# Performance work log

Measured on AMD Instinct MI355X. Metric: run time of the kernel, lower is better.

## Reference

```python
import jax, jax.numpy as jnp
import numpy as np

N = 100000  # nodes
E = 1600000  # directed edges

_DIMS = [("eg1", 3, 160), ("eg2", 160, 80), ("eg3", 80, 40), ("eg4", 40, 20),
         ("el1", 20, 10), ("el2", 10, 3), ("dl1", 3, 10), ("dl2", 10, 20),
         ("dg1", 20, 40), ("dg2", 40, 80), ("dg3", 80, 160), ("dg4", 160, 3)]


def _lin_init(key, ci, co):
    s = 1.0 / np.sqrt(ci)
    kw, kb = jax.random.split(key)
    w = jax.random.uniform(kw, (ci, co), jnp.float32, -s, s)
    b = jax.random.uniform(kb, (co,), jnp.float32, -s, s)
    return w, b


def setup_inputs():
    key = jax.random.key(0)
    k0, k1, k2 = jax.random.split(key, 3)
    x = jax.random.normal(k0, (N, 3), jnp.float32)
    src = jax.random.randint(k1, (E,), 0, N)
    dst = jax.random.randint(k2, (E,), 0, N)
    edge_index = jnp.stack([src, dst])  # [2, E] int32 indices
    out = {"x": x, "edge_index": edge_index}
    for i, (name, ci, co) in enumerate(_DIMS):
        w, b = _lin_init(jax.random.fold_in(key, i + 10), ci, co)
        out[name + "_w"] = w
        out[name + "_b"] = b
    return out


def _gcn(x, w, b, src, dst, norm):
    # PyG GCNConv: linear transform, then symmetric-normalized scatter-add.
    h = x @ w
    agg = jax.ops.segment_sum(h[src] * norm[:, None], dst, num_segments=N)
    return agg + b


def reference(x, edge_index, eg1_w, eg1_b, eg2_w, eg2_b, eg3_w, eg3_b, eg4_w, eg4_b,
              el1_w, el1_b, el2_w, el2_b, dl1_w, dl1_b, dl2_w, dl2_b,
              dg1_w, dg1_b, dg2_w, dg2_b, dg3_w, dg3_b, dg4_w, dg4_b):
    loops = jnp.arange(N)
    src = jnp.concatenate([edge_index[0], loops])  # add self-loops (PyG default)
    dst = jnp.concatenate([edge_index[1], loops])
    deg = jax.ops.segment_sum(jnp.ones(src.shape[0], x.dtype), dst, num_segments=N)
    dis = jnp.where(deg > 0, jax.lax.rsqrt(deg), 0.0)
    norm = dis[src] * dis[dst]  # D^-1/2 A D^-1/2 edge weights
    relu = jax.nn.relu
    h = relu(_gcn(x, eg1_w, eg1_b, src, dst, norm))
    h = relu(_gcn(h, eg2_w, eg2_b, src, dst, norm))
    h = relu(_gcn(h, eg3_w, eg3_b, src, dst, norm))
    h = relu(_gcn(h, eg4_w, eg4_b, src, dst, norm))
    h = relu(h @ el1_w + el1_b)
    h = h @ el2_w + el2_b  # latent [N, 3]
    h = relu(h @ dl1_w + dl1_b)
    h = relu(h @ dl2_w + dl2_b)
    h = relu(_gcn(h, dg1_w, dg1_b, src, dst, norm))
    h = relu(_gcn(h, dg2_w, dg2_b, src, dst, norm))
    h = relu(_gcn(h, dg3_w, dg3_b, src, dst, norm))
    h = jnp.tanh(_gcn(h, dg4_w, dg4_b, src, dst, norm))
    return h
```

## Files before the change

### kernel.cpp

```cpp
#include <hip/hip_runtime.h>
#include <hip/hip_fp16.h>
#include <math.h>

#define BS 256
static constexpr int NN = 100000;
static constexpr int EE = 1600000;
static constexpr int BUCKET_SH = 7;
static constexpr int NBUCKET = (NN + 127) >> BUCKET_SH;
static constexpr int NB_PART = 256;
static constexpr int CHUNK = EE / NB_PART;
static constexpr int NP = NBUCKET * NB_PART;
static constexpr int SCAN_ELEMS = 1024;
static constexpr int NPB = (NP + SCAN_ELEMS - 1) / SCAN_ELEMS;

static inline int cdiv(long long a, int b) { return (int)((a + b - 1) / b); }

template <int ACT>
__device__ __forceinline__ float act_f(float v) {
    if (ACT == 1) return fmaxf(v, 0.0f);
    if (ACT == 2) return tanhf(v);
    return v;
}

__device__ __forceinline__ unsigned short h16(float v) {
    return __half_as_ushort(__float2half(v));
}
__device__ __forceinline__ unsigned pack2h(float a, float b) {
    return (unsigned)h16(a) | ((unsigned)h16(b) << 16);
}
__device__ __forceinline__ float4 cvt4h(uint2 r) {
    float2 fa = __half22float2(*(const __half2*)&r.x);
    float2 fb = __half22float2(*(const __half2*)&r.y);
    return make_float4(fa.x, fa.y, fb.x, fb.y);
}
__device__ __forceinline__ void acc8h(uint4 r, float4& a, float4& b) {
    float2 f0 = __half22float2(*(const __half2*)&r.x);
    float2 f1 = __half22float2(*(const __half2*)&r.y);
    float2 f2 = __half22float2(*(const __half2*)&r.z);
    float2 f3 = __half22float2(*(const __half2*)&r.w);
    a.x += f0.x; a.y += f0.y; a.z += f1.x; a.w += f1.y;
    b.x += f2.x; b.y += f2.y; b.z += f3.x; b.w += f3.y;
}

template <int OUTM>
__device__ __forceinline__ void store1(float* out, size_t idx, float v, float dn) {
    if (OUTM == 0) out[idx] = v;
    else if (OUTM == 1) out[idx] = v * dn;
    else if (OUTM == 2) ((unsigned short*)out)[idx] = h16(v * dn);
    else ((unsigned short*)out)[idx] = h16(v);
}

__global__ __launch_bounds__(256) void k_hist(const int* __restrict__ dst,
                                              int* __restrict__ part_cnt) {
    __shared__ int h[NBUCKET];
    int b = blockIdx.x;
    for (int j = threadIdx.x; j < NBUCKET; j += 256) h[j] = 0;
    __syncthreads();
    int e0 = b * CHUNK;
    for (int k = threadIdx.x; k < CHUNK; k += 256)
        atomicAdd(&h[dst[e0 + k] >> BUCKET_SH], 1);
    __syncthreads();
    for (int j = threadIdx.x; j < NBUCKET; j += 256)
        part_cnt[j * NB_PART + b] = h[j];
}

__global__ void k_scanA(const int* __restrict__ in, int* __restrict__ outp,
                        int* __restrict__ bsums) {
    __shared__ int lds[BS];
    int base = blockIdx.x * SCAN_ELEMS;
    int t = threadIdx.x;
    int v[4];
    int s = 0;
#pragma unroll
    for (int j = 0; j < 4; ++j) {
        int idx = base + t * 4 + j;
        v[j] = (idx < NP) ? in[idx] : 0;
        s += v[j];
    }
    lds[t] = s;
    __syncthreads();
    for (int off = 1; off < BS; off <<= 1) {
        int add = (t >= off) ? lds[t - off] : 0;
        __syncthreads();
        lds[t] += add;
        __syncthreads();
    }
    int run = lds[t] - s;
    if (t == BS - 1) bsums[blockIdx.x] = lds[BS - 1];
#pragma unroll
    for (int j = 0; j < 4; ++j) {
        int idx = base + t * 4 + j;
        if (idx < NP) outp[idx] = run;
        run += v[j];
    }
}

__global__ void k_scanB(int* __restrict__ bsums) {
    if (threadIdx.x == 0 && blockIdx.x == 0) {
        int acc = 0;
        for (int i = 0; i < NPB; ++i) {
            int t = bsums[i];
            bsums[i] = acc;
            acc += t;
        }
    }
}

__global__ void k_scanC(int* __restrict__ outp, const int* __restrict__ bsums,
                        int* __restrict__ bbase) {
    int i = blockIdx.x * BS + threadIdx.x;
    if (i < NP) {
        int v = outp[i] + bsums[i / SCAN_ELEMS];
        outp[i] = v;
        if ((i & (NB_PART - 1)) == 0) bbase[i / NB_PART] = v;
    }
    if (i == 0) bbase[NBUCKET] = EE;
}

__global__ __launch_bounds__(256) void k_part(const int* __restrict__ src,
                                              const int* __restrict__ dst,
                                              const int* __restrict__ scan_out,
                                              unsigned* __restrict__ epb) {
    __shared__ int cur[NBUCKET];
    int b = blockIdx.x;
    for (int j = threadIdx.x; j < NBUCKET; j += 256) cur[j] = scan_out[j * NB_PART + b];
    __syncthreads();
    int e0 = b * CHUNK;
    for (int k = threadIdx.x; k < CHUNK; k += 256) {
        int e = e0 + k;
        int d = dst[e];
        int s = src[e];
        int pos = atomicAdd(&cur[d >> BUCKET_SH], 1);
        epb[pos] = ((unsigned)(d & ((1 << BUCKET_SH) - 1)) << 17) | (unsigned)s;
    }
}

__global__ __launch_bounds__(256) void k_fine2(const int* __restrict__ bbase,
                                               const unsigned* __restrict__ epb,
                                               int* __restrict__ eidx,
                                               int* __restrict__ rowptr,
                                               float* __restrict__ dis) {
    __shared__ int hcnt[1 << BUCKET_SH];
    __shared__ int hoff[1 << BUCKET_SH];
    int b = blockIdx.x;
    int n0 = b << BUCKET_SH;
    int nloc = min(1 << BUCKET_SH, NN - n0);
    int t = threadIdx.x;
    if (t < (1 << BUCKET_SH)) hcnt[t] = 0;
    __syncthreads();
    int es = bbase[b], ee = bbase[b + 1];
    for (int k = es + t; k < ee; k += 256) atomicAdd(&hcnt[epb[k] >> 17], 1);
    __syncthreads();
    if (t < (1 << BUCKET_SH)) hoff[t] = hcnt[t];
    __syncthreads();
    for (int off = 1; off < (1 << BUCKET_SH); off <<= 1) {
        int add = (t >= off && t < (1 << BUCKET_SH)) ? hoff[t - off] : 0;
        __syncthreads();
        if (t < (1 << BUCKET_SH)) hoff[t] += add;
        __syncthreads();
    }
    if (t < nloc) {
        int excl = hoff[t] - hcnt[t];
        rowptr[n0 + t] = es + excl;
        dis[n0 + t] = rsqrtf((float)(hcnt[t] + 1));
    }
    __syncthreads();
    if (t < (1 << BUCKET_SH)) hoff[t] = es + hoff[t] - hcnt[t];
    __syncthreads();
    for (int k = es + t; k < ee; k += 256) {
        unsigned p = epb[k];
        int pos = atomicAdd(&hoff[p >> 17], 1);
        eidx[pos] = (int)(p & 0x1FFFFu);
    }
    if (b == NBUCKET - 1 && t == 0) rowptr[NN] = EE;
}

template <int C, int ACT, bool HASB, bool OUTH>
__global__ void k_gatherw(const unsigned short* __restrict__ g, const int* __restrict__ rowptr,
                          const int* __restrict__ eidx, const float* __restrict__ dis,
                          const float* __restrict__ b, float* __restrict__ out) {
    static_assert(C % 8 == 0, "C%8");
    constexpr int V = C / 8;
    int t = blockIdx.x * BS + threadIdx.x;
    if (t >= NN * V) return;
    int n = t / V, v = t % V;
    const uint4* g4 = (const uint4*)g;
    float4 accA = make_float4(0.f, 0.f, 0.f, 0.f);
    float4 accB = make_float4(0.f, 0.f, 0.f, 0.f);
    acc8h(g4[(size_t)n * V + v], accA, accB);
    int rs = rowptr[n], re = rowptr[n + 1];
    int k = rs;
    for (; k + 4 <= re; k += 4) {
        int s0 = eidx[k + 0], s1 = eidx[k + 1], s2 = eidx[k + 2], s3 = eidx[k + 3];
        uint4 r0 = g4[(size_t)s0 * V + v];
        uint4 r1 = g4[(size_t)s1 * V + v];
        uint4 r2 = g4[(size_t)s2 * V + v];
        uint4 r3 = g4[(size_t)s3 * V + v];
        acc8h(r0, accA, accB);
        acc8h(r1, accA, accB);
        acc8h(r2, accA, accB);
        acc8h(r3, accA, accB);
    }
    for (; k < re; ++k) {
        acc8h(g4[(size_t)eidx[k] * V + v], accA, accB);
    }
    float dn = dis[n];
    accA.x *= dn; accA.y *= dn; accA.z *= dn; accA.w *= dn;
    accB.x *= dn; accB.y *= dn; accB.z *= dn; accB.w *= dn;
    if (HASB) {
        float4 b0 = ((const float4*)b)[v * 2 + 0];
        float4 b1 = ((const float4*)b)[v * 2 + 1];
        accA.x += b0.x; accA.y += b0.y; accA.z += b0.z; accA.w += b0.w;
        accB.x += b1.x; accB.y += b1.y; accB.z += b1.z; accB.w += b1.w;
    }
    accA.x = act_f<ACT>(accA.x); accA.y = act_f<ACT>(accA.y);
    accA.z = act_f<ACT>(accA.z); accA.w = act_f<ACT>(accA.w);
    accB.x = act_f<ACT>(accB.x); accB.y = act_f<ACT>(accB.y);
    accB.z = act_f<ACT>(accB.z); accB.w = act_f<ACT>(accB.w);
    if (OUTH) {
        uint4 u;
        u.x = pack2h(accA.x, accA.y);
        u.y = pack2h(accA.z, accA.w);
        u.z = pack2h(accB.x, accB.y);
        u.w = pack2h(accB.z, accB.w);
        ((uint4*)out)[(size_t)n * V + v] = u;
    } else {
        float4* op = (float4*)out + (size_t)n * (C / 4) + v * 2;
        op[0] = accA;
        op[1] = accB;
    }
}

template <int C, int ACT, bool HASB, bool OUTH>
__global__ void k_gatherh(const unsigned short* __restrict__ g, const int* __restrict__ rowptr,
                          const int* __restrict__ eidx, const float* __restrict__ dis,
                          const float* __restrict__ b, float* __restrict__ out) {
    static_assert(C % 4 == 0, "C%4");
    constexpr int V = C / 4;
    int t = blockIdx.x * BS + threadIdx.x;
    if (t >= NN * V) return;
    int n = t / V, v = t % V;
    const uint2* g2 = (const uint2*)g;
    float4 acc = cvt4h(g2[(size_t)n * V + v]);
    int rs = rowptr[n], re = rowptr[n + 1];
    int k = rs;
    for (; k + 4 <= re; k += 4) {
        int s0 = eidx[k + 0], s1 = eidx[k + 1], s2 = eidx[k + 2], s3 = eidx[k + 3];
        uint2 r0 = g2[(size_t)s0 * V + v];
        uint2 r1 = g2[(size_t)s1 * V + v];
        uint2 r2 = g2[(size_t)s2 * V + v];
        uint2 r3 = g2[(size_t)s3 * V + v];
        float4 h0 = cvt4h(r0), h1 = cvt4h(r1), h2 = cvt4h(r2), h3 = cvt4h(r3);
        acc.x += (h0.x + h1.x) + (h2.x + h3.x);
        acc.y += (h0.y + h1.y) + (h2.y + h3.y);
        acc.z += (h0.z + h1.z) + (h2.z + h3.z);
        acc.w += (h0.w + h1.w) + (h2.w + h3.w);
    }
    for (; k < re; ++k) {
        float4 hv = cvt4h(g2[(size_t)eidx[k] * V + v]);
        acc.x += hv.x; acc.y += hv.y; acc.z += hv.z; acc.w += hv.w;
    }
    float dn = dis[n];
    acc.x *= dn; acc.y *= dn; acc.z *= dn; acc.w *= dn;
    if (HASB) {
        float4 bb = ((const float4*)b)[v];
        acc.x += bb.x; acc.y += bb.y; acc.z += bb.z; acc.w += bb.w;
    }
    acc.x = act_f<ACT>(acc.x);
    acc.y = act_f<ACT>(acc.y);
    acc.z = act_f<ACT>(acc.z);
    acc.w = act_f<ACT>(acc.w);
    if (OUTH) {
        uint2 u;
        u.x = pack2h(acc.x, acc.y);
        u.y = pack2h(acc.z, acc.w);
        ((uint2*)out)[(size_t)n * V + v] = u;
    } else {
        ((float4*)out)[(size_t)n * V + v] = acc;
    }
}

template <int ACT, bool HASB>
__global__ void k_gather3d(const float* __restrict__ g, const int* __restrict__ rowptr,
                           const int* __restrict__ eidx, const float* __restrict__ dis,
                           const float* __restrict__ b, float* __restrict__ out) {
    int n = blockIdx.x * BS + threadIdx.x;
    if (n >= NN) return;
    const float* gp = g + (size_t)n * 3;
    float a0 = gp[0], a1 = gp[1], a2 = gp[2];
    int rs = rowptr[n], re = rowptr[n + 1];
    int k = rs;
    for (; k + 4 <= re; k += 4) {
        const float* q0 = g + (size_t)eidx[k + 0] * 3;
        const float* q1 = g + (size_t)eidx[k + 1] * 3;
        const float* q2 = g + (size_t)eidx[k + 2] * 3;
        const float* q3 = g + (size_t)eidx[k + 3] * 3;
        float b00 = q0[0], b01 = q0[1], b02 = q0[2];
        float b10 = q1[0], b11 = q1[1], b12 = q1[2];
        float b20 = q2[0], b21 = q2[1], b22 = q2[2];
        float b30 = q3[0], b31 = q3[1], b32 = q3[2];
        a0 += (b00 + b10) + (b20 + b30);
        a1 += (b01 + b11) + (b21 + b31);
        a2 += (b02 + b12) + (b22 + b32);
    }
    for (; k < re; ++k) {
        const float* gq = g + (size_t)eidx[k] * 3;
        a0 += gq[0]; a1 += gq[1]; a2 += gq[2];
    }
    float dn = dis[n];
    a0 *= dn; a1 *= dn; a2 *= dn;
    if (HASB) { a0 += b[0]; a1 += b[1]; a2 += b[2]; }
    float* op = out + (size_t)n * 3;
    op[0] = act_f<ACT>(a0);
    op[1] = act_f<ACT>(a1);
    op[2] = act_f<ACT>(a2);
}

__global__ void k_scale3(const float* __restrict__ x, const float* __restrict__ dis,
                         float* __restrict__ g) {
    int i = blockIdx.x * BS + threadIdx.x;
    if (i < NN * 3) g[i] = x[i] * dis[i / 3];
}

__global__ __launch_bounds__(256) void k_latent(const unsigned short* __restrict__ in20,
                                                const float* __restrict__ el1_w, const float* __restrict__ el1_b,
                                                const float* __restrict__ el2_w, const float* __restrict__ el2_b,
                                                const float* __restrict__ dl1_w, const float* __restrict__ dl1_b,
                                                const float* __restrict__ dl2_w, const float* __restrict__ dl2_b,
                                                const float* __restrict__ dis,
                                                unsigned short* __restrict__ G) {
    __shared__ float w1[200], b1[10], w2[30], b2[3], w3[30], b3[10], w4[200], b4[20];
    int t = threadIdx.x;
    if (t < 200) w1[t] = el1_w[t];
    if (t < 10) b1[t] = el1_b[t];
    if (t < 30) w2[t] = el2_w[t];
    if (t < 3) b2[t] = el2_b[t];
    if (t < 30) w3[t] = dl1_w[t];
    if (t < 10) b3[t] = dl1_b[t];
    if (t < 200) w4[t] = dl2_w[t];
    if (t < 20) b4[t] = dl2_b[t];
    __syncthreads();
    int n = blockIdx.x * 256 + t;
    if (n >= NN) return;
    float h0[20];
    const uint2* ip = (const uint2*)in20 + (size_t)n * 5;
#pragma unroll
    for (int v = 0; v < 5; ++v) {
        float4 f = cvt4h(ip[v]);
        h0[v * 4 + 0] = f.x; h0[v * 4 + 1] = f.y;
        h0[v * 4 + 2] = f.z; h0[v * 4 + 3] = f.w;
    }
    float a1[10];
#pragma unroll
    for (int j = 0; j < 10; ++j) {
        float s = b1[j];
#pragma unroll
        for (int i = 0; i < 20; ++i) s = fmaf(h0[i], w1[i * 10 + j], s);
        a1[j] = fmaxf(s, 0.0f);
    }
    float a2[3];
#pragma unroll
    for (int j = 0; j < 3; ++j) {
        float s = b2[j];
#pragma unroll
        for (int i = 0; i < 10; ++i) s = fmaf(a1[i], w2[i * 3 + j], s);
        a2[j] = s;
    }
    float a3[10];
#pragma unroll
    for (int j = 0; j < 10; ++j) {
        float s = b3[j];
#pragma unroll
        for (int i = 0; i < 3; ++i) s = fmaf(a2[i], w3[i * 10 + j], s);
        a3[j] = fmaxf(s, 0.0f);
    }
    float dn = dis[n];
    uint2* gp = (uint2*)G + (size_t)n * 5;
#pragma unroll
    for (int v = 0; v < 5; ++v) {
        float o[4];
#pragma unroll
        for (int q = 0; q < 4; ++q) {
            int j = v * 4 + q;
            float s = b4[j];
#pragma unroll
            for (int i = 0; i < 10; ++i) s = fmaf(a3[i], w4[i * 20 + j], s);
            o[q] = fmaxf(s, 0.0f) * dn;
        }
        uint2 u;
        u.x = pack2h(o[0], o[1]);
        u.y = pack2h(o[2], o[3]);
        gp[v] = u;
    }
}

template <int CIN, int COUT, int TC, int TN, int TM, int BK, int ACT, bool HASB, int OUTM, bool INH>
__global__ __launch_bounds__(256) void k_mm_tiled(const float* __restrict__ x,
                                                  const float* __restrict__ w,
                                                  const float* __restrict__ b,
                                                  float* __restrict__ out,
                                                  const float* __restrict__ dis) {
    constexpr int TR = 256 / TC;
    constexpr int BM = TR * TM;
    constexpr int LDA = BM + 4;
    constexpr int CHUNKS = CIN / BK;
    constexpr int BK4 = BK / 4;
    constexpr int CIN4 = CIN / 4;
    static_assert(TC * TN == COUT, "cols");
    static_assert(CIN % BK == 0 && BK % 4 == 0, "bk");
    static_assert(TM == 4 || TM == 8, "tm");
    __shared__ float As[BK * LDA];
    __shared__ float Ws[BK * COUT];
    const int tid = threadIdx.x;
    const int tc = tid % TC, tr = tid / TC;
    const int n0 = blockIdx.x * BM;

    float acc[TM][TN];
#pragma unroll
    for (int r = 0; r < TM; ++r)
#pragma unroll
        for (int j = 0; j < TN; ++j) acc[r][j] = HASB ? b[tc * TN + j] : 0.0f;

    const float4* x4 = (const float4*)x;
    const uint2* xh = (const uint2*)x;
    const float4* w4 = (const float4*)w;

    for (int ch = 0; ch < CHUNKS; ++ch) {
        const int kb4 = ch * BK4;
        if (ch) __syncthreads();
        for (int i = tid; i < BM * BK4; i += 256) {
            int r = i / BK4, k4 = i % BK4;
            int row = n0 + r;
            float4 v = make_float4(0.f, 0.f, 0.f, 0.f);
            if (row < NN) {
                if (INH) v = cvt4h(xh[(size_t)row * CIN4 + kb4 + k4]);
                else v = x4[(size_t)row * CIN4 + kb4 + k4];
            }
            int base = (4 * k4) * LDA + r;
            As[base] = v.x;
            As[base + LDA] = v.y;
            As[base + 2 * LDA] = v.z;
            As[base + 3 * LDA] = v.w;
        }
        for (int i = tid; i < BK * COUT / 4; i += 256) {
            ((float4*)Ws)[i] = w4[(size_t)kb4 * COUT + i];
        }
        __syncthreads();
#pragma unroll 4
        for (int k = 0; k < BK; ++k) {
            float a[TM];
            *(float4*)&a[0] = *(const float4*)&As[k * LDA + tr * TM];
            if (TM == 8) *(float4*)&a[4] = *(const float4*)&As[k * LDA + tr * TM + 4];
            float wr[TN];
#pragma unroll
            for (int j = 0; j < TN; ++j) wr[j] = Ws[k * COUT + tc * TN + j];
#pragma unroll
            for (int r = 0; r < TM; ++r)
#pragma unroll
                for (int j = 0; j < TN; ++j) acc[r][j] = fmaf(a[r], wr[j], acc[r][j]);
        }
    }
#pragma unroll
    for (int r = 0; r < TM; ++r) {
        int row = n0 + tr * TM + r;
        if (row < NN) {
            float dn = (OUTM == 1 || OUTM == 2) ? dis[row] : 0.0f;
            size_t base = (size_t)row * COUT + tc * TN;
#pragma unroll
            for (int j = 0; j < TN; ++j) store1<OUTM>(out, base + j, act_f<ACT>(acc[r][j]), dn);
        }
    }
}

template <int CIN, int COUT, int ACT, bool HASB, int OUTM, bool INH>
__global__ void k_mm_vec4(const float* __restrict__ x, const float* __restrict__ w,
                          const float* __restrict__ b, float* __restrict__ out,
                          const float* __restrict__ dis) {
    static_assert(CIN % 4 == 0 && COUT % 4 == 0, "align");
    constexpr int TM = 8;
    constexpr int CIN4 = CIN / 4;
    constexpr int COUT4 = COUT / 4;
    constexpr int RG = NN / TM;
    int i = blockIdx.x * BS + threadIdx.x;
    if (i >= RG * COUT4) return;
    int c4 = i % COUT4;
    int n0 = (i / COUT4) * TM;
    const float4* x4 = (const float4*)x;
    const uint2* xh = (const uint2*)x;
    const float4* w4 = (const float4*)w;
    float4 acc[TM];
    float4 bb = HASB ? ((const float4*)b)[c4] : make_float4(0.f, 0.f, 0.f, 0.f);
#pragma unroll
    for (int r = 0; r < TM; ++r) acc[r] = bb;
    for (int k4 = 0; k4 < CIN4; ++k4) {
        float4 wv[4];
#pragma unroll
        for (int j = 0; j < 4; ++j) wv[j] = w4[(size_t)(4 * k4 + j) * COUT4 + c4];
#pragma unroll
        for (int r = 0; r < TM; ++r) {
            float4 xv;
            if (INH) xv = cvt4h(xh[(size_t)(n0 + r) * CIN4 + k4]);
            else xv = x4[(size_t)(n0 + r) * CIN4 + k4];
            acc[r].x = fmaf(xv.x, wv[0].x, fmaf(xv.y, wv[1].x, fmaf(xv.z, wv[2].x, fmaf(xv.w, wv[3].x, acc[r].x))));
            acc[r].y = fmaf(xv.x, wv[0].y, fmaf(xv.y, wv[1].y, fmaf(xv.z, wv[2].y, fmaf(xv.w, wv[3].y, acc[r].y))));
            acc[r].z = fmaf(xv.x, wv[0].z, fmaf(xv.y, wv[1].z, fmaf(xv.z, wv[2].z, fmaf(xv.w, wv[3].z, acc[r].z))));
            acc[r].w = fmaf(xv.x, wv[0].w, fmaf(xv.y, wv[1].w, fmaf(xv.z, wv[2].w, fmaf(xv.w, wv[3].w, acc[r].w))));
        }
    }
#pragma unroll
    for (int r = 0; r < TM; ++r) {
        float vx = act_f<ACT>(acc[r].x), vy = act_f<ACT>(acc[r].y);
        float vz = act_f<ACT>(acc[r].z), vw = act_f<ACT>(acc[r].w);
        size_t gi = (size_t)(n0 + r) * COUT4 + c4;
        if (OUTM == 2) {
            float dn = dis[n0 + r];
            uint2 u;
            u.x = pack2h(vx * dn, vy * dn);
            u.y = pack2h(vz * dn, vw * dn);
            ((uint2*)out)[gi] = u;
        } else if (OUTM == 1) {
            float dn = dis[n0 + r];
            ((float4*)out)[gi] = make_float4(vx * dn, vy * dn, vz * dn, vw * dn);
        } else {
            ((float4*)out)[gi] = make_float4(vx, vy, vz, vw);
        }
    }
}

template <int CIN, int COUT, int ACT, int OUTM>
__global__ void k_mm_rowbcast(const float* __restrict__ x, const float* __restrict__ w,
                              const float* __restrict__ b, float* __restrict__ out) {
    static_assert(COUT % 4 == 0, "c4");
    constexpr int COUT4 = COUT / 4;
    int i = blockIdx.x * BS + threadIdx.x;
    if (i >= NN * COUT4) return;
    int n = i / COUT4, c4 = i % COUT4;
    const float4* w4 = (const float4*)w;
    float4 acc = ((const float4*)b)[c4];
    const float* xr = x + (size_t)n * CIN;
#pragma unroll
    for (int ci = 0; ci < CIN; ++ci) {
        float xv = xr[ci];
        float4 wv = w4[ci * COUT4 + c4];
        acc.x = fmaf(xv, wv.x, acc.x);
        acc.y = fmaf(xv, wv.y, acc.y);
        acc.z = fmaf(xv, wv.z, acc.z);
        acc.w = fmaf(xv, wv.w, acc.w);
    }
    acc.x = act_f<ACT>(acc.x); acc.y = act_f<ACT>(acc.y);
    acc.z = act_f<ACT>(acc.z); acc.w = act_f<ACT>(acc.w);
    if (OUTM == 3) {
        uint2 u;
        u.x = pack2h(acc.x, acc.y);
        u.y = pack2h(acc.z, acc.w);
        ((uint2*)out)[(size_t)n * COUT4 + c4] = u;
    } else {
        ((float4*)out)[(size_t)n * COUT4 + c4] = acc;
    }
}

template <int CIN, int COUT, int ACT, bool HASB, int OUTM, bool INH>
__global__ void k_mm_vec(const float* __restrict__ x, const float* __restrict__ w,
                         const float* __restrict__ b, float* __restrict__ out,
                         const float* __restrict__ dis) {
    static_assert(CIN % 4 == 0, "CIN%4");
    constexpr int TM = 8;
    constexpr int CIN4 = CIN / 4;
    constexpr int RG = NN / TM;
    int i = blockIdx.x * BS + threadIdx.x;
    if (i >= RG * COUT) return;
    int c = i % COUT;
    int n0 = (i / COUT) * TM;
    float acc[TM];
    float bb = HASB ? b[c] : 0.0f;
#pragma unroll
    for (int r = 0; r < TM; ++r) acc[r] = bb;
    const float4* x4 = (const float4*)x;
    const uint2* xh = (const uint2*)x;
    for (int k = 0; k < CIN4; ++k) {
        float w0 = w[(4 * k + 0) * COUT + c];
        float w1 = w[(4 * k + 1) * COUT + c];
        float w2 = w[(4 * k + 2) * COUT + c];
        float w3 = w[(4 * k + 3) * COUT + c];
#pragma unroll
        for (int r = 0; r < TM; ++r) {
            float4 xv;
            if (INH) xv = cvt4h(xh[(size_t)(n0 + r) * CIN4 + k]);
            else xv = x4[(size_t)(n0 + r) * CIN4 + k];
            acc[r] = fmaf(xv.x, w0, fmaf(xv.y, w1, fmaf(xv.z, w2, fmaf(xv.w, w3, acc[r]))));
        }
    }
#pragma unroll
    for (int r = 0; r < TM; ++r) {
        int row = n0 + r;
        float dn = (OUTM == 1 || OUTM == 2) ? dis[row] : 0.0f;
        store1<OUTM>(out, (size_t)row * COUT + c, act_f<ACT>(acc[r]), dn);
    }
}

extern "C" void kernel_launch(void* const* d_in, const int* in_sizes, int n_in,
                              void* d_out, int out_size, void* d_ws, size_t ws_size,
                              hipStream_t stream) {
    const float* x = (const float*)d_in[0];
    const int* ei = (const int*)d_in[1];
    const int* src = ei;
    const int* dst = ei + EE;
    const float* eg1_w = (const float*)d_in[2];  const float* eg1_b = (const float*)d_in[3];
    const float* eg2_w = (const float*)d_in[4];  const float* eg2_b = (const float*)d_in[5];
    const float* eg3_w = (const float*)d_in[6];  const float* eg3_b = (const float*)d_in[7];
    const float* eg4_w = (const float*)d_in[8];  const float* eg4_b = (const float*)d_in[9];
    const float* el1_w = (const float*)d_in[10]; const float* el1_b = (const float*)d_in[11];
    const float* el2_w = (const float*)d_in[12]; const float* el2_b = (const float*)d_in[13];
    const float* dl1_w = (const float*)d_in[14]; const float* dl1_b = (const float*)d_in[15];
    const float* dl2_w = (const float*)d_in[16]; const float* dl2_b = (const float*)d_in[17];
    const float* dg1_w = (const float*)d_in[18]; const float* dg1_b = (const float*)d_in[19];
    const float* dg2_w = (const float*)d_in[20]; const float* dg2_b = (const float*)d_in[21];
    const float* dg3_w = (const float*)d_in[22]; const float* dg3_b = (const float*)d_in[23];
    const float* dg4_w = (const float*)d_in[24]; const float* dg4_b = (const float*)d_in[25];
    float* out = (float*)d_out;

    char* ws = (char*)d_ws;
    size_t off = 0;
    auto alloc = [&](size_t bytes) {
        void* p = ws + off;
        off += (bytes + 15) & ~(size_t)15;
        return p;
    };
    int* part_cnt = (int*)alloc(sizeof(int) * NP);
    int* scan_out = (int*)alloc(sizeof(int) * NP);
    int* bsums    = (int*)alloc(sizeof(int) * NPB);
    int* bbase    = (int*)alloc(sizeof(int) * (NBUCKET + 1));
    int* rowptr   = (int*)alloc(sizeof(int) * (NN + 1));
    float* dis    = (float*)alloc(sizeof(float) * NN);
    int* eidx     = (int*)alloc(sizeof(int) * EE);
    unsigned* epb = (unsigned*)alloc(sizeof(unsigned) * EE);
    unsigned short* G = (unsigned short*)alloc(sizeof(unsigned short) * 80 * (size_t)NN);
    float* bufA = (float*)alloc(sizeof(float) * 160 * (size_t)NN);
    float* bufB = (float*)alloc(sizeof(float) * 160 * (size_t)NN);

    k_hist<<<NB_PART, 256, 0, stream>>>(dst, part_cnt);
    k_scanA<<<NPB, BS, 0, stream>>>(part_cnt, scan_out, bsums);
    k_scanB<<<1, 64, 0, stream>>>(bsums);
    k_scanC<<<cdiv(NP, BS), BS, 0, stream>>>(scan_out, bsums, bbase);
    k_part<<<NB_PART, 256, 0, stream>>>(src, dst, scan_out, epb);
    k_fine2<<<NBUCKET, 256, 0, stream>>>(bbase, epb, eidx, rowptr, dis);

    k_scale3<<<cdiv(3LL * NN, BS), BS, 0, stream>>>(x, dis, bufB);
    k_gather3d<0, false><<<cdiv(NN, BS), BS, 0, stream>>>(bufB, rowptr, eidx, dis, nullptr, bufA);
    k_mm_rowbcast<3, 160, 1, 3><<<cdiv(NN * 40LL, BS), BS, 0, stream>>>(bufA, eg1_w, eg1_b, bufB);

    k_mm_tiled<160, 80, 16, 5, 8, 32, 0, false, 2, true><<<cdiv(NN, 128), 256, 0, stream>>>(
        bufB, eg2_w, nullptr, (float*)G, dis);
    k_gatherw<80, 1, true, true><<<cdiv(NN * 10LL, BS), BS, 0, stream>>>(G, rowptr, eidx, dis, eg2_b, bufA);

    k_mm_tiled<80, 40, 8, 5, 4, 40, 0, false, 2, true><<<cdiv(NN, 128), 256, 0, stream>>>(
        bufA, eg3_w, nullptr, (float*)G, dis);
    k_gatherw<40, 1, true, true><<<cdiv(NN * 5LL, BS), BS, 0, stream>>>(G, rowptr, eidx, dis, eg3_b, bufB);

    k_mm_vec4<40, 20, 0, false, 2, true><<<cdiv((NN / 8) * 5LL, BS), BS, 0, stream>>>(
        bufB, eg4_w, nullptr, (float*)G, dis);
    k_gatherh<20, 1, true, true><<<cdiv(NN * 5LL, BS), BS, 0, stream>>>(G, rowptr, eidx, dis, eg4_b, bufA);

    k_latent<<<cdiv(NN, 256), 256, 0, stream>>>((const unsigned short*)bufA,
        el1_w, el1_b, el2_w, el2_b, dl1_w, dl1_b, dl2_w, dl2_b, dis, G);

    k_gatherh<20, 0, false, true><<<cdiv(NN * 5LL, BS), BS, 0, stream>>>(G, rowptr, eidx, dis, nullptr, bufA);
    k_mm_vec4<20, 40, 1, true, 2, true><<<cdiv((NN / 8) * 10LL, BS), BS, 0, stream>>>(
        bufA, dg1_w, dg1_b, (float*)G, dis);

    k_gatherw<40, 0, false, true><<<cdiv(NN * 5LL, BS), BS, 0, stream>>>(G, rowptr, eidx, dis, nullptr, bufB);
    k_mm_tiled<40, 80, 16, 5, 8, 40, 1, true, 2, true><<<cdiv(NN, 128), 256, 0, stream>>>(
        bufB, dg2_w, dg2_b, (float*)G, dis);

    k_gatherw<80, 0, false, true><<<cdiv(NN * 10LL, BS), BS, 0, stream>>>(G, rowptr, eidx, dis, nullptr, bufA);
    k_mm_tiled<80, 160, 32, 5, 8, 40, 1, true, 3, true><<<cdiv(NN, 64), 256, 0, stream>>>(
        bufA, dg3_w, dg3_b, bufB, nullptr);

    k_mm_vec<160, 3, 0, false, 1, true><<<cdiv((NN / 8) * 3LL, BS), BS, 0, stream>>>(bufB, dg4_w, nullptr, bufA, dis);
    k_gather3d<2, true><<<cdiv(NN, BS), BS, 0, stream>>>(bufA, rowptr, eidx, dis, dg4_b, out);
}
```

Before: 593.2 us.

## Replace FP32 tiled matmuls with fp16 MFMA 16x16x32 kernel

Adds a matrix-core GEMM kernel that loads fp16 activations and fp16-converted weights into LDS and uses mfma_f32_16x16x32_f16 with fp32 accumulation. It replaces the four scalar-FMA tiled matmul calls for the 160/80/40-wide layers. The goal is to move the dense per-node transforms off the vector ALUs onto the matrix cores. The costs are that weights are converted to fp16, which adds rounding, and that every block reconverts and reloads the whole weight matrix into LDS. Output stores are scalar 16-bit writes, which may not coalesce well.

```diff
diff --git a/kernel.cpp b/kernel.cpp
--- a/kernel.cpp
+++ b/kernel.cpp
@@ -9,11 +9,14 @@
 static constexpr int NBUCKET = (NN + 127) >> BUCKET_SH;
 static constexpr int NB_PART = 256;
 static constexpr int CHUNK = EE / NB_PART;
-static constexpr int NP = NBUCKET * NB_PART;
+static constexpr int NP_ = NBUCKET * NB_PART;
 static constexpr int SCAN_ELEMS = 1024;
-static constexpr int NPB = (NP + SCAN_ELEMS - 1) / SCAN_ELEMS;
+static constexpr int NPB = (NP_ + SCAN_ELEMS - 1) / SCAN_ELEMS;
 
 static inline int cdiv(long long a, int b) { return (int)((a + b - 1) / b); }
+
+typedef _Float16 half8 __attribute__((ext_vector_type(8)));
+typedef float f32x4 __attribute__((ext_vector_type(4)));
 
 template <int ACT>
 __device__ __forceinline__ float act_f(float v) {
@@ -74,7 +77,7 @@
 #pragma unroll
     for (int j = 0; j < 4; ++j) {
         int idx = base + t * 4 + j;
-        v[j] = (idx < NP) ? in[idx] : 0;
+        v[j] = (idx < NP_) ? in[idx] : 0;
         s += v[j];
     }
     lds[t] = s;
@@ -90,7 +93,7 @@
 #pragma unroll
     for (int j = 0; j < 4; ++j) {
         int idx = base + t * 4 + j;
-        if (idx < NP) outp[idx] = run;
+        if (idx < NP_) outp[idx] = run;
         run += v[j];
     }
 }
@@ -109,7 +112,7 @@
 __global__ void k_scanC(int* __restrict__ outp, const int* __restrict__ bsums,
                         int* __restrict__ bbase) {
     int i = blockIdx.x * BS + threadIdx.x;
-    if (i < NP) {
+    if (i < NP_) {
         int v = outp[i] + bsums[i / SCAN_ELEMS];
         outp[i] = v;
         if ((i & (NB_PART - 1)) == 0) bbase[i / NB_PART] = v;
@@ -394,81 +397,106 @@
     }
 }
 
-template <int CIN, int COUT, int TC, int TN, int TM, int BK, int ACT, bool HASB, int OUTM, bool INH>
-__global__ __launch_bounds__(256) void k_mm_tiled(const float* __restrict__ x,
-                                                  const float* __restrict__ w,
-                                                  const float* __restrict__ b,
-                                                  float* __restrict__ out,
-                                                  const float* __restrict__ dis) {
-    constexpr int TR = 256 / TC;
-    constexpr int BM = TR * TM;
-    constexpr int LDA = BM + 4;
-    constexpr int CHUNKS = CIN / BK;
-    constexpr int BK4 = BK / 4;
-    constexpr int CIN4 = CIN / 4;
-    static_assert(TC * TN == COUT, "cols");
-    static_assert(CIN % BK == 0 && BK % 4 == 0, "bk");
-    static_assert(TM == 4 || TM == 8, "tm");
-    __shared__ float As[BK * LDA];
-    __shared__ float Ws[BK * COUT];
+template <int K, int N, int ACT, bool HASB, int OUTM>
+__global__ __launch_bounds__(256) void k_mm_mfma(const unsigned short* __restrict__ x,
+                                                 const float* __restrict__ w,
+                                                 const float* __restrict__ bias,
+                                                 unsigned short* __restrict__ out,
+                                                 const float* __restrict__ dis) {
+    constexpr int KP = (K + 31) & ~31;
+    constexpr int NT = (N + 15) / 16;
+    constexpr int NPAD = NT * 16;
+    constexpr int KC = KP / 32;
+    constexpr int SP = KP + 8;
+    __shared__ _Float16 Al[64 * SP];
+    __shared__ _Float16 Wl[(KP / 8) * NPAD * 8];
     const int tid = threadIdx.x;
-    const int tc = tid % TC, tr = tid / TC;
-    const int n0 = blockIdx.x * BM;
-
-    float acc[TM][TN];
-#pragma unroll
-    for (int r = 0; r < TM; ++r)
-#pragma unroll
-        for (int j = 0; j < TN; ++j) acc[r][j] = HASB ? b[tc * TN + j] : 0.0f;
-
-    const float4* x4 = (const float4*)x;
-    const uint2* xh = (const uint2*)x;
+    const int n0 = blockIdx.x * 64;
+
+    {
+        constexpr int K4 = KP / 4;
+        const uint2* x2 = (const uint2*)x;
+        for (int i = tid; i < 64 * K4; i += 256) {
+            int r = i / K4, k4 = i % K4;
+            uint2 v = make_uint2(0u, 0u);
+            int row = n0 + r;
+            if (row < NN && k4 * 4 < K) v = x2[(size_t)row * (K / 4) + k4];
+            *(uint2*)&Al[r * SP + k4 * 4] = v;
+        }
+    }
+    for (int i = tid; i < KP * NPAD; i += 256) {
+        int k = i / NPAD, n = i % NPAD;
+        float v = (k < K && n < N) ? w[k * N + n] : 0.0f;
+        Wl[(k >> 3) * NPAD * 8 + n * 8 + (k & 7)] = (_Float16)v;
+    }
+    __syncthreads();
+
+    const int wave = tid >> 6;
+    const int lane = tid & 63;
+    const int lm = lane & 15;
+    const int quad = lane >> 4;
+
+    f32x4 acc[NT];
+#pragma unroll
+    for (int t = 0; t < NT; ++t) acc[t] = (f32x4){0.f, 0.f, 0.f, 0.f};
+
+    const int arow = wave * 16 + lm;
+#pragma unroll
+    for (int kc = 0; kc < KC; ++kc) {
+        half8 a = *(const half8*)&Al[arow * SP + kc * 32 + quad * 8];
+#pragma unroll
+        for (int t = 0; t < NT; ++t) {
+            half8 bf = *(const half8*)&Wl[(kc * 4 + quad) * NPAD * 8 + (t * 16 + lm) * 8];
+            acc[t] = __builtin_amdgcn_mfma_f32_16x16x32_f16(a, bf, acc[t], 0, 0, 0);
+        }
+    }
+#pragma unroll
+    for (int t = 0; t < NT; ++t) {
+        int col = t * 16 + lm;
+        if (col < N) {
+            float bb = HASB ? bias[col] : 0.0f;
+#pragma unroll
+            for (int r = 0; r < 4; ++r) {
+                int row = n0 + wave * 16 + quad * 4 + r;
+                if (row < NN) {
+                    float v = act_f<ACT>(acc[t][r] + bb);
+                    if (OUTM == 2) v *= dis[row];
+                    out[(size_t)row * N + col] = h16(v);
+                }
+            }
+        }
+    }
+}
+
+template <int CIN, int COUT, int ACT, int OUTM>
+__global__ void k_mm_rowbcast(const float* __restrict__ x, const float* __restrict__ w,
+                              const float* __restrict__ b, float* __restrict__ out) {
+    static_assert(COUT % 4 == 0, "c4");
+    constexpr int COUT4 = COUT / 4;
+    int i = blockIdx.x * BS + threadIdx.x;
+    if (i >= NN * COUT4) return;
+    int n = i / COUT4, c4 = i % COUT4;
     const float4* w4 = (const float4*)w;
-
-    for (int ch = 0; ch < CHUNKS; ++ch) {
-        const int kb4 = ch * BK4;
-        if (ch) __syncthreads();
-        for (int i = tid; i < BM * BK4; i += 256) {
-            int r = i / BK4, k4 = i % BK4;
-            int row = n0 + r;
-            float4 v = make_float4(0.f, 0.f, 0.f, 0.f);
-            if (row < NN) {
-                if (INH) v = cvt4h(xh[(size_t)row * CIN4 + kb4 + k4]);
-                else v = x4[(size_t)row * CIN4 + kb4 + k4];
-            }
-            int base = (4 * k4) * LDA + r;
-            As[base] = v.x;
-            As[base + LDA] = v.y;
-            As[base + 2 * LDA] = v.z;
-            As[base + 3 * LDA] = v.w;
-        }
-        for (int i = tid; i < BK * COUT / 4; i += 256) {
-            ((float4*)Ws)[i] = w4[(size_t)kb4 * COUT + i];
-        }
-        __syncthreads();
-#pragma unroll 4
-        for (int k = 0; k < BK; ++k) {
-            float a[TM];
-            *(float4*)&a[0] = *(const float4*)&As[k * LDA + tr * TM];
-            if (TM == 8) *(float4*)&a[4] = *(const float4*)&As[k * LDA + tr * TM + 4];
-            float wr[TN];
-#pragma unroll
-            for (int j = 0; j < TN; ++j) wr[j] = Ws[k * COUT + tc * TN + j];
-#pragma unroll
-            for (int r = 0; r < TM; ++r)
-#pragma unroll
-                for (int j = 0; j < TN; ++j) acc[r][j] = fmaf(a[r], wr[j], acc[r][j]);
-        }
-    }
-#pragma unroll
-    for (int r = 0; r < TM; ++r) {
-        int row = n0 + tr * TM + r;
-        if (row < NN) {
-            float dn = (OUTM == 1 || OUTM == 2) ? dis[row] : 0.0f;
-            size_t base = (size_t)row * COUT + tc * TN;
-#pragma unroll
-            for (int j = 0; j < TN; ++j) store1<OUTM>(out, base + j, act_f<ACT>(acc[r][j]), dn);
-        }
+    float4 acc = ((const float4*)b)[c4];
+    const float* xr = x + (size_t)n * CIN;
+#pragma unroll
+    for (int ci = 0; ci < CIN; ++ci) {
+        float xv = xr[ci];
+        float4 wv = w4[ci * COUT4 + c4];
+        acc.x = fmaf(xv, wv.x, acc.x);
+        acc.y = fmaf(xv, wv.y, acc.y);
+        acc.z = fmaf(xv, wv.z, acc.z);
+        acc.w = fmaf(xv, wv.w, acc.w);
+    }
+    acc.x = act_f<ACT>(acc.x); acc.y = act_f<ACT>(acc.y);
+    acc.z = act_f<ACT>(acc.z); acc.w = act_f<ACT>(acc.w);
+    if (OUTM == 3) {
+        uint2 u;
+        u.x = pack2h(acc.x, acc.y);
+        u.y = pack2h(acc.z, acc.w);
+        ((uint2*)out)[(size_t)n * COUT4 + c4] = u;
+    } else {
+        ((float4*)out)[(size_t)n * COUT4 + c4] = acc;
     }
 }
 
@@ -524,38 +552,6 @@
         } else {
             ((float4*)out)[gi] = make_float4(vx, vy, vz, vw);
         }
-    }
-}
-
-template <int CIN, int COUT, int ACT, int OUTM>
-__global__ void k_mm_rowbcast(const float* __restrict__ x, const float* __restrict__ w,
-                              const float* __restrict__ b, float* __restrict__ out) {
-    static_assert(COUT % 4 == 0, "c4");
-    constexpr int COUT4 = COUT / 4;
-    int i = blockIdx.x * BS + threadIdx.x;
-    if (i >= NN * COUT4) return;
-    int n = i / COUT4, c4 = i % COUT4;
-    const float4* w4 = (const float4*)w;
-    float4 acc = ((const float4*)b)[c4];
-    const float* xr = x + (size_t)n * CIN;
-#pragma unroll
-    for (int ci = 0; ci < CIN; ++ci) {
-        float xv = xr[ci];
-        float4 wv = w4[ci * COUT4 + c4];
-        acc.x = fmaf(xv, wv.x, acc.x);
-        acc.y = fmaf(xv, wv.y, acc.y);
-        acc.z = fmaf(xv, wv.z, acc.z);
-        acc.w = fmaf(xv, wv.w, acc.w);
-    }
-    acc.x = act_f<ACT>(acc.x); acc.y = act_f<ACT>(acc.y);
-    acc.z = act_f<ACT>(acc.z); acc.w = act_f<ACT>(acc.w);
-    if (OUTM == 3) {
-        uint2 u;
-        u.x = pack2h(acc.x, acc.y);
-        u.y = pack2h(acc.z, acc.w);
-        ((uint2*)out)[(size_t)n * COUT4 + c4] = u;
-    } else {
-        ((float4*)out)[(size_t)n * COUT4 + c4] = acc;
     }
 }
 
@@ -626,8 +622,8 @@
         off += (bytes + 15) & ~(size_t)15;
         return p;
     };
-    int* part_cnt = (int*)alloc(sizeof(int) * NP);
-    int* scan_out = (int*)alloc(sizeof(int) * NP);
+    int* part_cnt = (int*)alloc(sizeof(int) * NP_);
+    int* scan_out = (int*)alloc(sizeof(int) * NP_);
     int* bsums    = (int*)alloc(sizeof(int) * NPB);
     int* bbase    = (int*)alloc(sizeof(int) * (NBUCKET + 1));
     int* rowptr   = (int*)alloc(sizeof(int) * (NN + 1));
@@ -641,7 +637,7 @@
     k_hist<<<NB_PART, 256, 0, stream>>>(dst, part_cnt);
     k_scanA<<<NPB, BS, 0, stream>>>(part_cnt, scan_out, bsums);
     k_scanB<<<1, 64, 0, stream>>>(bsums);
-    k_scanC<<<cdiv(NP, BS), BS, 0, stream>>>(scan_out, bsums, bbase);
+    k_scanC<<<cdiv(NP_, BS), BS, 0, stream>>>(scan_out, bsums, bbase);
     k_part<<<NB_PART, 256, 0, stream>>>(src, dst, scan_out, epb);
     k_fine2<<<NBUCKET, 256, 0, stream>>>(bbase, epb, eidx, rowptr, dis);
 
@@ -649,12 +645,12 @@
     k_gather3d<0, false><<<cdiv(NN, BS), BS, 0, stream>>>(bufB, rowptr, eidx, dis, nullptr, bufA);
     k_mm_rowbcast<3, 160, 1, 3><<<cdiv(NN * 40LL, BS), BS, 0, stream>>>(bufA, eg1_w, eg1_b, bufB);
 
-    k_mm_tiled<160, 80, 16, 5, 8, 32, 0, false, 2, true><<<cdiv(NN, 128), 256, 0, stream>>>(
-        bufB, eg2_w, nullptr, (float*)G, dis);
+    k_mm_mfma<160, 80, 0, false, 2><<<cdiv(NN, 64), 256, 0, stream>>>(
+        (const unsigned short*)bufB, eg2_w, nullptr, G, dis);
     k_gatherw<80, 1, true, true><<<cdiv(NN * 10LL, BS), BS, 0, stream>>>(G, rowptr, eidx, dis, eg2_b, bufA);
 
-    k_mm_tiled<80, 40, 8, 5, 4, 40, 0, false, 2, true><<<cdiv(NN, 128), 256, 0, stream>>>(
-        bufA, eg3_w, nullptr, (float*)G, dis);
+    k_mm_mfma<80, 40, 0, false, 2><<<cdiv(NN, 64), 256, 0, stream>>>(
+        (const unsigned short*)bufA, eg3_w, nullptr, G, dis);
     k_gatherw<40, 1, true, true><<<cdiv(NN * 5LL, BS), BS, 0, stream>>>(G, rowptr, eidx, dis, eg3_b, bufB);
 
     k_mm_vec4<40, 20, 0, false, 2, true><<<cdiv((NN / 8) * 5LL, BS), BS, 0, stream>>>(
@@ -669,12 +665,12 @@
         bufA, dg1_w, dg1_b, (float*)G, dis);
 
     k_gatherw<40, 0, false, true><<<cdiv(NN * 5LL, BS), BS, 0, stream>>>(G, rowptr, eidx, dis, nullptr, bufB);
-    k_mm_tiled<40, 80, 16, 5, 8, 40, 1, true, 2, true><<<cdiv(NN, 128), 256, 0, stream>>>(
-        bufB, dg2_w, dg2_b, (float*)G, dis);
+    k_mm_mfma<40, 80, 1, true, 2><<<cdiv(NN, 64), 256, 0, stream>>>(
+        (const unsigned short*)bufB, dg2_w, dg2_b, G, dis);
 
     k_gatherw<80, 0, false, true><<<cdiv(NN * 10LL, BS), BS, 0, stream>>>(G, rowptr, eidx, dis, nullptr, bufA);
-    k_mm_tiled<80, 160, 32, 5, 8, 40, 1, true, 3, true><<<cdiv(NN, 64), 256, 0, stream>>>(
-        bufA, dg3_w, dg3_b, bufB, nullptr);
+    k_mm_mfma<80, 160, 1, true, 3><<<cdiv(NN, 64), 256, 0, stream>>>(
+        (const unsigned short*)bufA, dg3_w, dg3_b, (unsigned short*)bufB, nullptr);
 
     k_mm_vec<160, 3, 0, false, 1, true><<<cdiv((NN / 8) * 3LL, BS), BS, 0, stream>>>(bufB, dg4_w, nullptr, bufA, dis);
     k_gather3d<2, true><<<cdiv(NN, BS), BS, 0, stream>>>(bufA, rowptr, eidx, dis, dg4_b, out);
```

New measurement: 593.3 us. No clear change (+0.0%).
